# Performance work log

Hardware: AMD Instinct MI355X
Metric: run time of the kernel (lower is better)

The kernel has to match this reference:

```python
import jax, jax.numpy as jnp
import numpy as np

H, W, P, U = 32, 32, 64, 64
KB = KC = KD = 3
L, BSZ = 32, 8


def conv2d(x, k):
    # x: (N,H,W,Cin), k: (kh,kw,Cin,Cout), SAME padding, stride 1
    return jax.lax.conv_general_dilated(
        x, k, (1, 1), 'SAME', dimension_numbers=('NHWC', 'HWIO', 'NHWC'))


def dst_Q(N):
    # skew DST eigenbasis: Q[i,j] = i^(i+1) * sin(pi (i+1)(j+1)/(N+1)) / sqrt((N+1)/2)
    idx = jnp.arange(1, N + 1, dtype=jnp.float32)
    S = jnp.sin(jnp.pi * idx[:, None] * idx[None, :] / (N + 1)) / jnp.sqrt((N + 1) / 2.0)
    phase = jnp.exp(1j * (jnp.pi / 2.0) * idx)  # i^(i+1)
    return (phase[:, None] * S.astype(jnp.complex64)).astype(jnp.complex64)


def make_basis_skew(N, M):
    ih = jnp.arange(1, N + 1, dtype=jnp.float32)
    iw = jnp.arange(1, M + 1, dtype=jnp.float32)
    ch = 2.0 * jnp.cos(jnp.pi * ih / (N + 1))  # (N,)
    cw = 2.0 * jnp.cos(jnp.pi * iw / (M + 1))  # (M,)
    b = jnp.broadcast_to(cw[None, :], (N, M)).reshape(-1)
    c = jnp.broadcast_to(ch[:, None], (N, M)).reshape(-1)
    d = (ch[:, None] * cw[None, :]).reshape(-1)
    return jnp.stack((b, c, d), axis=-1)  # (N*M, 3)


def setup_inputs() -> dict:
    key = jax.random.key(0)
    ks = jax.random.split(key, 12)
    dt_min, dt_max = 0.001, 0.1
    inp = {
        'input_sequence': jax.random.normal(ks[0], (L, BSZ, H, W, U), dtype=jnp.float32),
        'x0': jax.random.normal(ks[1], (BSZ, H, W, U), dtype=jnp.float32),
        'Lambda_re': -(jax.random.uniform(ks[2], (P,), dtype=jnp.float32) * 0.9 + 0.1),
        'Lambda_im': jnp.pi * jnp.arange(P, dtype=jnp.float32),
        'values': jnp.zeros((P, 4), dtype=jnp.float32),
        'log_step': jax.random.uniform(ks[3], (P,), dtype=jnp.float32)
                    * (np.log(dt_max) - np.log(dt_min)) + np.log(dt_min),
        'B_r': jax.random.normal(ks[4], (KB, KB, U, P), dtype=jnp.float32) * np.sqrt(2.0 / (U * KB * KB)),
        'B_i': jax.random.normal(ks[5], (KB, KB, U, P), dtype=jnp.float32) * np.sqrt(2.0 / (U * KB * KB)),
        'C_r': jax.random.normal(ks[6], (KC, KC, P, U), dtype=jnp.float32) * np.sqrt(2.0 / (2 * P * KC * KC)),
        'C_i': jax.random.normal(ks[7], (KC, KC, P, U), dtype=jnp.float32) * np.sqrt(2.0 / (2 * P * KC * KC)),
        'D_kernel': jax.random.normal(ks[8], (KD, KD, U, U), dtype=jnp.float32) * np.sqrt(2.0 / (U * KD * KD)),
    }
    return inp


def reference(input_sequence, x0, Lambda_re, Lambda_im, values, log_step,
              B_r, B_i, C_r, C_i, D_kernel):
    Lq, Bq = input_sequence.shape[0], input_sequence.shape[1]
    # ---- diagonal state matrix (clip_eigs=True) ----
    Lambda = (jnp.minimum(Lambda_re, -1e-4) + 1j * Lambda_im).astype(jnp.complex64)  # (P,)
    # ---- diagonalized BTST spectrum D via skew basis ----
    basis = make_basis_skew(H, W).astype(jnp.complex64)  # (HW,3)
    v = jax.nn.softmax(values, axis=-1) * 4.0
    xk, yk, zk, wk = v[:, 0], v[:, 1], v[:, 2], v[:, 3]
    kv = jnp.stack(((xk + yk - 2) / 4, (xk + zk - 2) / 4, (xk + wk - 2) / 8), axis=-1).astype(jnp.complex64)
    D = jnp.einsum('pn,hn->ph', kv, basis) + 1.0  # (P, HW)
    # ---- ZOH discretization ----
    step = jnp.exp(log_step)  # (P,)
    temp = Lambda[:, None] * D  # (P, HW)
    A_bar = jnp.exp(temp * step[:, None])
    B_coeff = (A_bar - 1.0) / temp
    A_bar = A_bar.T.reshape(H, W, P)      # (H,W,P)
    B_coeff = B_coeff.T.reshape(H, W, P)  # (H,W,P)
    # ---- DST eigenbases ----
    Qh = dst_Q(H); Qw = dst_Q(W)
    Qh_inv = jnp.conj(Qh).T; Qw_inv = jnp.conj(Qw).T
    # ---- input path: B conv then transform to eigen domain ----
    u = input_sequence.reshape(Lq * Bq, H, W, U)
    Bu = (conv2d(u, B_r) + 1j * conv2d(u, B_i)).reshape(Lq, Bq, H, W, P)
    Bu_hat = jnp.einsum('ah,lbhwp,cw->lbacp', Qh_inv, Bu, Qw_inv)
    b_elems = B_coeff * Bu_hat  # (L,B,H,W,P)
    # ---- initial state from x0 through the same B path ----
    Bx0 = conv2d(x0, B_r) + 1j * conv2d(x0, B_i)  # (B,H,W,P)
    x0_hat = jnp.einsum('ah,bhwp,cw->bacp', Qh_inv, Bx0, Qw_inv) * B_coeff
    b_elems = b_elems.at[0].add(A_bar * x0_hat)
    # ---- parallel linear recurrence x_k = A_bar*x_{k-1} + b_k ----
    A_elems = jnp.broadcast_to(A_bar.astype(jnp.complex64), b_elems.shape)
    def binop(e1, e2):
        a1, b1 = e1; a2, b2 = e2
        return (a2 * a1, a2 * b1 + b2)
    _, xs = jax.lax.associative_scan(binop, (A_elems, b_elems), axis=0)
    # ---- back to spatial domain, C projection (2*Re), D feedthrough ----
    x_sp = jnp.einsum('ha,lbacp,wc->lbhwp', Qh, xs, Qw)  # (L,B,H,W,P) complex
    xr = x_sp.real.reshape(Lq * Bq, H, W, P)
    xi = x_sp.imag.reshape(Lq * Bq, H, W, P)
    y = 2.0 * (conv2d(xr, C_r) - conv2d(xi, C_i))  # Re(x @ C_tilde)
    y = y + conv2d(u, D_kernel)
    y = jax.nn.gelu(y)
    return y.reshape(Lq, Bq, H, W, U)
```

## Files before the change

kernel.cpp:

```cpp
#include <hip/hip_runtime.h>
#include <cmath>

#ifndef M_PI
#define M_PI 3.14159265358979323846
#endif

#define NH 32
#define NW 32
#define NP 64
#define NU 64
#define NL 32
#define NB 8
#define NIMG 256
#define NIMG_TOT 264
#define HWN 1024
#define IMG_STRIDE 65536

typedef unsigned short u16;
typedef unsigned int u32;
typedef __bf16 bf16x8 __attribute__((ext_vector_type(8)));
typedef float f32x4 __attribute__((ext_vector_type(4)));

__device__ __forceinline__ u16 f2bf(float f) {
  unsigned u = __float_as_uint(f);
  u += 0x7fffu + ((u >> 16) & 1u);
  return (u16)(u >> 16);
}
__device__ __forceinline__ float bf2f(u16 h) {
  return __uint_as_float(((unsigned)h) << 16);
}


__global__ void k_setup(const float* __restrict__ values, float* __restrict__ S,
                        float* __restrict__ kv) {
  int t = threadIdx.x;
  int i = t >> 5, j = t & 31;
  double s = sin(M_PI * (double)((i + 1) * (j + 1)) / 33.0) / sqrt(16.5);
  S[t] = (float)s;
  if (t < NP) {
    float v0 = values[t * 4 + 0], v1 = values[t * 4 + 1];
    float v2 = values[t * 4 + 2], v3 = values[t * 4 + 3];
    float m = fmaxf(fmaxf(v0, v1), fmaxf(v2, v3));
    float e0 = expf(v0 - m), e1 = expf(v1 - m), e2 = expf(v2 - m), e3 = expf(v3 - m);
    float inv = 4.0f / (e0 + e1 + e2 + e3);
    float xk = e0 * inv, yk = e1 * inv, zk = e2 * inv, wk = e3 * inv;
    kv[t * 4 + 0] = (xk + yk - 2.0f) * 0.25f;
    kv[t * 4 + 1] = (xk + zk - 2.0f) * 0.25f;
    kv[t * 4 + 2] = (xk + wk - 2.0f) * 0.125f;
    kv[t * 4 + 3] = 0.f;
  }
}

__global__ void k_coeff(const float* __restrict__ Lre, const float* __restrict__ Lim,
                        const float* __restrict__ log_step, const float* __restrict__ kv,
                        float2* __restrict__ A, float2* __restrict__ Bc) {
  int tid = blockIdx.x * blockDim.x + threadIdx.x;
  int n = tid >> 6, p = tid & 63;
  int h = n >> 5, w = n & 31;
  double ch = 2.0 * cos(M_PI * (double)(h + 1) / 33.0);
  double cw = 2.0 * cos(M_PI * (double)(w + 1) / 33.0);
  double Dv = (double)kv[p * 4 + 0] * cw + (double)kv[p * 4 + 1] * ch +
              (double)kv[p * 4 + 2] * ch * cw + 1.0;
  double lr = fmin((double)Lre[p], -0.0001);
  double li = (double)Lim[p];
  double tr = lr * Dv, ti = li * Dv;
  double st = exp((double)log_step[p]);
  double zr = tr * st, zi = ti * st;
  double ea = exp(zr);
  double Ar = ea * cos(zi), Ai = ea * sin(zi);
  double d = tr * tr + ti * ti;
  double br = ((Ar - 1.0) * tr + Ai * ti) / d;
  double bi = (Ai * tr - (Ar - 1.0) * ti) / d;
  size_t o = (size_t)(p >> 1) * 2048 + (size_t)n * 2 + (p & 1);
  A[o]  = make_float2((float)Ar, (float)Ai);
  Bc[o] = make_float2((float)br, (float)bi);
}

#define NB_PACK (18 * 8 * 64 * 8)
#define NC_PACK (54 * 4 * 64 * 8)
__global__ __launch_bounds__(256) void k_pack(
    const float* __restrict__ Br, const float* __restrict__ Bi,
    const float* __restrict__ Cr, const float* __restrict__ Ci,
    const float* __restrict__ Dk,
    u16* __restrict__ WBhi, u16* __restrict__ WBlo,
    u16* __restrict__ WChi, u16* __restrict__ WClo) {
  int tid = blockIdx.x * 256 + threadIdx.x;
  if (tid < NB_PACK) {
    int j = tid & 7, lane = (tid >> 3) & 63, nt = (tid >> 9) & 7, kc = tid >> 12;
    int k = kc * 32 + ((lane >> 4) << 3) + j;
    int n = nt * 16 + (lane & 15);
    int tap = k >> 6, c = k & 63;
    float w = (n < 64) ? Br[(tap * 64 + c) * 64 + n]
                       : Bi[(tap * 64 + c) * 64 + (n - 64)];
    u16 hi = f2bf(w);
    WBhi[tid] = hi;
    WBlo[tid] = f2bf(w - bf2f(hi));
  } else {
    int t2 = tid - NB_PACK;
    if (t2 < NC_PACK) {
      int j = t2 & 7, lane = (t2 >> 3) & 63, nt = (t2 >> 9) & 3, kc = t2 >> 11;
      int k = kc * 32 + ((lane >> 4) << 3) + j;
      int n = nt * 16 + (lane & 15);
      int s = k / 576, rem = k % 576;
      int tap = rem >> 6, c = rem & 63;
      int widx = (tap * 64 + c) * 64 + n;
      float w = (s == 0) ? 2.f * Cr[widx] : (s == 1) ? -2.f * Ci[widx] : Dk[widx];
      u16 hi = f2bf(w);
      WChi[t2] = hi;
      WClo[t2] = f2bf(w - bf2f(hi));
    }
  }
}

__global__ __launch_bounds__(256) void k_convB_mfma(
    const float* __restrict__ u, const float* __restrict__ x0,
    const u16* __restrict__ WBhi, const u16* __restrict__ WBlo,
    float2* __restrict__ XBUF) {
  __shared__ u16 lhs[6 * 34 * 64];
  __shared__ u16 lls[6 * 34 * 64];
  int img = blockIdx.x, h0 = blockIdx.y * 4;
  int t = threadIdx.x;
  const float* src = (img < NIMG) ? (u + (size_t)img * HWN * NU)
                                  : (x0 + (size_t)(img - NIMG) * HWN * NU);
  for (int z = t; z < 6 * 2 * 32; z += 256) {
    int col = z & 31, rw = z >> 5;
    int r = rw >> 1, w = (rw & 1) * 33;
    ((u32*)&lhs[(r * 34 + w) * 64])[col] = 0;
    ((u32*)&lls[(r * 34 + w) * 64])[col] = 0;
  }
  for (int idx = t; idx < 6 * 32 * 16; idx += 256) {
    int c4 = idx & 15, wi = (idx >> 4) & 31, r = idx >> 9;
    int hh = h0 - 1 + r;
    float4 v = make_float4(0.f, 0.f, 0.f, 0.f);
    if (hh >= 0 && hh < NH)
      v = *(const float4*)(src + (hh * 32 + wi) * 64 + c4 * 4);
    u16 a0 = f2bf(v.x), a1 = f2bf(v.y), a2 = f2bf(v.z), a3 = f2bf(v.w);
    u16 b0 = f2bf(v.x - bf2f(a0)), b1 = f2bf(v.y - bf2f(a1));
    u16 b2 = f2bf(v.z - bf2f(a2)), b3 = f2bf(v.w - bf2f(a3));
    int w = wi + 1;
    int a = (r * 34 + w) * 64 + (((c4 >> 1) ^ (w & 7)) << 3) + ((c4 & 1) << 2);
    *(ushort4*)&lhs[a] = make_ushort4(a0, a1, a2, a3);
    *(ushort4*)&lls[a] = make_ushort4(b0, b1, b2, b3);
  }
  __syncthreads();
  int lane = t & 63, wv = t >> 6;
  int mgrp = wv >> 1, ng = wv & 1;
  int l15 = lane & 15, l4 = lane >> 4;
  f32x4 acc[4][4];
#pragma unroll
  for (int i = 0; i < 4; i++)
#pragma unroll
    for (int q = 0; q < 4; q++) acc[i][q] = (f32x4){0.f, 0.f, 0.f, 0.f};

  for (int tap = 0; tap < 9; tap++) {
    int kh = tap / 3, kw = tap - kh * 3;
#pragma unroll
    for (int cc = 0; cc < 2; cc++) {
      int kc = tap * 2 + cc;
      bf16x8 ah[4], al[4], wh[4], wl[4];
#pragma unroll
      for (int mti = 0; mti < 4; mti++) {
        int row = mgrp * 2 + (mti >> 1);
        int wt = (mti & 1) * 16 + l15 + kw;
        int off = ((row + kh) * 34 + wt) * 64 + (((cc * 4 + l4) ^ (wt & 7)) << 3);
        ah[mti] = *(const bf16x8*)&lhs[off];
        al[mti] = *(const bf16x8*)&lls[off];
      }
#pragma unroll
      for (int q = 0; q < 4; q++) {
        int nt = ng * 2 + (q & 1) + (q >> 1) * 4;
        size_t woff = ((size_t)((kc * 8 + nt) * 64 + lane)) * 8;
        wh[q] = *(const bf16x8*)&WBhi[woff];
        wl[q] = *(const bf16x8*)&WBlo[woff];
      }
#pragma unroll
      for (int mti = 0; mti < 4; mti++)
#pragma unroll
        for (int q = 0; q < 4; q++) {
          f32x4 c = acc[mti][q];
          c = __builtin_amdgcn_mfma_f32_16x16x32_bf16(ah[mti], wh[q], c, 0, 0, 0);
          c = __builtin_amdgcn_mfma_f32_16x16x32_bf16(ah[mti], wl[q], c, 0, 0, 0);
          c = __builtin_amdgcn_mfma_f32_16x16x32_bf16(al[mti], wh[q], c, 0, 0, 0);
          acc[mti][q] = c;
        }
    }
  }
  float2* dst = XBUF + (size_t)img * IMG_STRIDE;
#pragma unroll
  for (int mti = 0; mti < 4; mti++) {
    int h = h0 + mgrp * 2 + (mti >> 1);
#pragma unroll
    for (int half = 0; half < 2; half++) {
      int p = ng * 32 + half * 16 + l15;
      int pc = p >> 1, pp = p & 1;
#pragma unroll
      for (int reg = 0; reg < 4; reg++) {
        int wpix = (mti & 1) * 16 + l4 * 4 + reg;
        float re = acc[mti][half][reg];
        float im = acc[mti][2 + half][reg];
        int m = (h + wpix + 2) & 3;
        float2 o;
        if (m == 0)      o = make_float2( re,  im);
        else if (m == 1) o = make_float2( im, -re);
        else if (m == 2) o = make_float2(-re, -im);
        else             o = make_float2(-im,  re);
        dst[(size_t)pc * 2048 + (h * 32 + wpix) * 2 + pp] = o;
      }
    }
  }
}

__global__ __launch_bounds__(256) void k_dst_fwd(float2* __restrict__ XBUF,
                                                 const float* __restrict__ S) {
  int img = blockIdx.x, pc = blockIdx.y;
  __shared__ float tin[32 * 32 * 4];
  __shared__ float t1 [32 * 32 * 4];
  int t = threadIdx.x;
  float2* base = XBUF + (size_t)img * IMG_STRIDE + (size_t)pc * 2048;
  for (int n = t; n < 1024; n += 256) {
    float4 v = *(const float4*)&base[n * 2];
    *(float4*)&tin[n * 4] = v;
  }
  __syncthreads();
  {
    int w = t & 31, ag = t >> 5;
    f32x4 acc[4];
#pragma unroll
    for (int i = 0; i < 4; i++) acc[i] = (f32x4){0.f, 0.f, 0.f, 0.f};
#pragma unroll 8
    for (int hh = 0; hh < 32; hh++) {
      f32x4 v = *(const f32x4*)&tin[(hh * 32 + w) * 4];
      f32x4 s4 = *(const f32x4*)&S[hh * 32 + ag * 4];
#pragma unroll
      for (int i = 0; i < 4; i++) acc[i] += s4[i] * v;
    }
    int wp = w ^ (ag & 7);
#pragma unroll
    for (int i = 0; i < 4; i++)
      *(f32x4*)&t1[((ag * 4 + i) * 32 + wp) * 4] = acc[i];
  }
  __syncthreads();
  {
    int pp = t & 1, cg = (t >> 1) & 15, ag = t >> 5;
    float acc[4][2][2];
#pragma unroll
    for (int i = 0; i < 4; i++)
#pragma unroll
      for (int j = 0; j < 2; j++) acc[i][j][0] = acc[i][j][1] = 0.f;
#pragma unroll 8
    for (int w = 0; w < 32; w++) {
      int wp = w ^ (ag & 7);
      float2 sc = *(const float2*)&S[w * 32 + cg * 2];
#pragma unroll
      for (int i = 0; i < 4; i++) {
        float2 tv = *(const float2*)&t1[((ag * 4 + i) * 32 + wp) * 4 + pp * 2];
        acc[i][0][0] = fmaf(tv.x, sc.x, acc[i][0][0]);
        acc[i][0][1] = fmaf(tv.y, sc.x, acc[i][0][1]);
        acc[i][1][0] = fmaf(tv.x, sc.y, acc[i][1][0]);
        acc[i][1][1] = fmaf(tv.y, sc.y, acc[i][1][1]);
      }
    }
#pragma unroll
    for (int i = 0; i < 4; i++)
#pragma unroll
      for (int j = 0; j < 2; j++) {
        int n = (ag * 4 + i) * 32 + cg * 2 + j;
        base[n * 2 + pp] = make_float2(acc[i][j][0], acc[i][j][1]);
      }
  }
}

__global__ __launch_bounds__(256) void k_scan(const float2* __restrict__ A,
                                              const float2* __restrict__ Bc,
                                              float2* __restrict__ X) {
  int gx = blockIdx.x;
  int b = gx >> 8, sl = gx & 255;
  int t = threadIdx.x;
  size_t off = (size_t)sl * 256 + t;
  float2 Av = A[off];
  float2 Bv = Bc[off];
  float2 v0 = X[(size_t)(NIMG + b) * IMG_STRIDE + off];
  float2 x;
  x.x = Bv.x * v0.x - Bv.y * v0.y;
  x.y = Bv.x * v0.y + Bv.y * v0.x;
#pragma unroll 4
  for (int l = 0; l < NL; l++) {
    size_t idx = (size_t)(l * NB + b) * IMG_STRIDE + off;
    float2 v = X[idx];
    float vr = Bv.x * v.x - Bv.y * v.y;
    float vi = Bv.x * v.y + Bv.y * v.x;
    float2 nx;
    nx.x = Av.x * x.x - Av.y * x.y + vr;
    nx.y = Av.x * x.y + Av.y * x.x + vi;
    x = nx;
    X[idx] = x;
  }
}

__global__ __launch_bounds__(256) void k_dst_inv(float2* __restrict__ XBUF,
                                                 const float* __restrict__ S) {
  int img = blockIdx.x, pc = blockIdx.y;
  __shared__ float tin[32 * 32 * 4];
  __shared__ float t1 [32 * 32 * 4];
  int t = threadIdx.x;
  float2* base = XBUF + (size_t)img * IMG_STRIDE + (size_t)pc * 2048;
  for (int n = t; n < 1024; n += 256) {
    float4 v = *(const float4*)&base[n * 2];
    *(float4*)&tin[n * 4] = v;
  }
  __syncthreads();
  {
    int c = t & 31, ag = t >> 5;
    f32x4 acc[4];
#pragma unroll
    for (int i = 0; i < 4; i++) acc[i] = (f32x4){0.f, 0.f, 0.f, 0.f};
#pragma unroll 8
    for (int a = 0; a < 32; a++) {
      f32x4 v = *(const f32x4*)&tin[(a * 32 + c) * 4];
      f32x4 s4 = *(const f32x4*)&S[a * 32 + ag * 4];
#pragma unroll
      for (int i = 0; i < 4; i++) acc[i] += s4[i] * v;
    }
    int cp = c ^ (ag & 7);
#pragma unroll
    for (int i = 0; i < 4; i++)
      *(f32x4*)&t1[((ag * 4 + i) * 32 + cp) * 4] = acc[i];
  }
  __syncthreads();
  {
    int pp = t & 1, wg = (t >> 1) & 15, ag = t >> 5;
    float acc[4][2][2];
#pragma unroll
    for (int i = 0; i < 4; i++)
#pragma unroll
      for (int j = 0; j < 2; j++) acc[i][j][0] = acc[i][j][1] = 0.f;
#pragma unroll 8
    for (int c = 0; c < 32; c++) {
      int cp = c ^ (ag & 7);
      float2 sc = *(const float2*)&S[c * 32 + wg * 2];
#pragma unroll
      for (int i = 0; i < 4; i++) {
        float2 tv = *(const float2*)&t1[((ag * 4 + i) * 32 + cp) * 4 + pp * 2];
        acc[i][0][0] = fmaf(tv.x, sc.x, acc[i][0][0]);
        acc[i][0][1] = fmaf(tv.y, sc.x, acc[i][0][1]);
        acc[i][1][0] = fmaf(tv.x, sc.y, acc[i][1][0]);
        acc[i][1][1] = fmaf(tv.y, sc.y, acc[i][1][1]);
      }
    }
    u32* gw = (u32*)(XBUF + (size_t)img * IMG_STRIDE) + (size_t)pc * 4096;
#pragma unroll
    for (int i = 0; i < 4; i++)
#pragma unroll
      for (int j = 0; j < 2; j++) {
        int h = ag * 4 + i, wpx = wg * 2 + j;
        float re = acc[i][j][0], im = acc[i][j][1];
        int m = (h + wpx + 2) & 3;
        float2 o;
        if (m == 0)      o = make_float2( re,  im);
        else if (m == 1) o = make_float2(-im,  re);
        else if (m == 2) o = make_float2(-re, -im);
        else             o = make_float2( im, -re);
        u16 hr = f2bf(o.x), lr = f2bf(o.x - bf2f(hr));
        u16 hm = f2bf(o.y), lm = f2bf(o.y - bf2f(hm));
        int pix = h * 32 + wpx;
        gw[pix * 4 + pp]     = (u32)hr | ((u32)lr << 16);
        gw[pix * 4 + 2 + pp] = (u32)hm | ((u32)lm << 16);
      }
  }
}

__global__ __launch_bounds__(256) void k_convCD_mfma(
    const u32* __restrict__ XP,
    const float* __restrict__ u,
    const u16* __restrict__ WChi, const u16* __restrict__ WClo,
    float* __restrict__ out) {
  __shared__ u16 lhs[6 * 34 * 64];
  __shared__ u16 lls[6 * 34 * 64];
  int img = blockIdx.x, h0 = blockIdx.y * 4;
  int t = threadIdx.x;
  int lane = t & 63, wv = t >> 6;
  int mgrp = wv >> 1, ng = wv & 1;
  int l15 = lane & 15, l4 = lane >> 4;
  const u32* xim = XP + (size_t)img * IMG_STRIDE * 2;
  const float* uim = u + (size_t)img * HWN * NU;
  f32x4 acc[4][2];
#pragma unroll
  for (int i = 0; i < 4; i++) {
    acc[i][0] = (f32x4){0.f, 0.f, 0.f, 0.f};
    acc[i][1] = (f32x4){0.f, 0.f, 0.f, 0.f};
  }
  for (int z = t; z < 6 * 2 * 32; z += 256) {
    int col = z & 31, rw = z >> 5;
    int r = rw >> 1, w = (rw & 1) * 33;
    ((u32*)&lhs[(r * 34 + w) * 64])[col] = 0;
    ((u32*)&lls[(r * 34 + w) * 64])[col] = 0;
  }

  for (int s = 0; s < 3; s++) {
    __syncthreads();
    if (s < 2) {
      for (int idx = t; idx < 6 * 32 * 32; idx += 256) {
        int wi = idx & 31, pc = (idx >> 5) & 31, r = idx >> 10;
        int hh = h0 - 1 + r;
        uint2 d = make_uint2(0u, 0u);
        if (hh >= 0 && hh < NH)
          d = *(const uint2*)(xim + (size_t)pc * 4096 + (hh * 32 + wi) * 4 + s * 2);
        u32 hip = (d.x & 0xffffu) | (d.y << 16);
        u32 lop = (d.x >> 16) | (d.y & 0xffff0000u);
        int w = wi + 1;
        int c = pc * 2;
        int a = (r * 34 + w) * 64 + (((c >> 3) ^ (w & 7)) << 3) + (c & 7);
        *(u32*)&lhs[a] = hip;
        *(u32*)&lls[a] = lop;
      }
    } else {
      for (int idx = t; idx < 6 * 32 * 16; idx += 256) {
        int c4 = idx & 15, wi = (idx >> 4) & 31, r = idx >> 9;
        int hh = h0 - 1 + r;
        float4 v = make_float4(0.f, 0.f, 0.f, 0.f);
        if (hh >= 0 && hh < NH)
          v = *(const float4*)(uim + (hh * 32 + wi) * 64 + c4 * 4);
        u16 a0 = f2bf(v.x), a1 = f2bf(v.y), a2 = f2bf(v.z), a3 = f2bf(v.w);
        u16 b0 = f2bf(v.x - bf2f(a0)), b1 = f2bf(v.y - bf2f(a1));
        u16 b2 = f2bf(v.z - bf2f(a2)), b3 = f2bf(v.w - bf2f(a3));
        int w = wi + 1;
        int a = (r * 34 + w) * 64 + (((c4 >> 1) ^ (w & 7)) << 3) + ((c4 & 1) << 2);
        *(ushort4*)&lhs[a] = make_ushort4(a0, a1, a2, a3);
        *(ushort4*)&lls[a] = make_ushort4(b0, b1, b2, b3);
      }
    }
    __syncthreads();
    for (int tap = 0; tap < 9; tap++) {
      int kh = tap / 3, kw = tap - kh * 3;
#pragma unroll
      for (int cc = 0; cc < 2; cc++) {
        int kc = (s * 9 + tap) * 2 + cc;
        bf16x8 ah[4], al[4], wh[2], wl[2];
#pragma unroll
        for (int mti = 0; mti < 4; mti++) {
          int row = mgrp * 2 + (mti >> 1);
          int wt = (mti & 1) * 16 + l15 + kw;
          int off = ((row + kh) * 34 + wt) * 64 + (((cc * 4 + l4) ^ (wt & 7)) << 3);
          ah[mti] = *(const bf16x8*)&lhs[off];
          al[mti] = *(const bf16x8*)&lls[off];
        }
#pragma unroll
        for (int q = 0; q < 2; q++) {
          int nt = ng * 2 + q;
          size_t woff = ((size_t)((kc * 4 + nt) * 64 + lane)) * 8;
          wh[q] = *(const bf16x8*)&WChi[woff];
          wl[q] = *(const bf16x8*)&WClo[woff];
        }
#pragma unroll
        for (int mti = 0; mti < 4; mti++)
#pragma unroll
          for (int q = 0; q < 2; q++) {
            f32x4 c = acc[mti][q];
            c = __builtin_amdgcn_mfma_f32_16x16x32_bf16(ah[mti], wh[q], c, 0, 0, 0);
            c = __builtin_amdgcn_mfma_f32_16x16x32_bf16(ah[mti], wl[q], c, 0, 0, 0);
            c = __builtin_amdgcn_mfma_f32_16x16x32_bf16(al[mti], wh[q], c, 0, 0, 0);
            acc[mti][q] = c;
          }
      }
    }
  }
  float* dst = out + (size_t)img * HWN * NU;
#pragma unroll
  for (int mti = 0; mti < 4; mti++) {
    int h = h0 + mgrp * 2 + (mti >> 1);
#pragma unroll
    for (int q = 0; q < 2; q++) {
      int un = (ng * 2 + q) * 16 + l15;
#pragma unroll
      for (int reg = 0; reg < 4; reg++) {
        int wpix = (mti & 1) * 16 + l4 * 4 + reg;
        float x = acc[mti][q][reg];
        float z = 0.7978845608028654f * (x + 0.044715f * x * x * x);
        float e = __expf(2.f * z);
        float th = 1.f - 2.f / (e + 1.f);
        dst[(h * 32 + wpix) * 64 + un] = 0.5f * x * (1.f + th);
      }
    }
  }
}

extern "C" void kernel_launch(void* const* d_in, const int* in_sizes, int n_in,
                              void* d_out, int out_size, void* d_ws, size_t ws_size,
                              hipStream_t stream) {
  const float* u        = (const float*)d_in[0];
  const float* x0       = (const float*)d_in[1];
  const float* Lre      = (const float*)d_in[2];
  const float* Lim      = (const float*)d_in[3];
  const float* values   = (const float*)d_in[4];
  const float* log_step = (const float*)d_in[5];
  const float* Br       = (const float*)d_in[6];
  const float* Bi       = (const float*)d_in[7];
  const float* Cr       = (const float*)d_in[8];
  const float* Ci       = (const float*)d_in[9];
  const float* Dk       = (const float*)d_in[10];
  float* out = (float*)d_out;

  char* ws = (char*)d_ws;
  float*  S    = (float*)ws;                       ws += 4096;
  float*  kv   = (float*)ws;                       ws += 4096;
  float2* A    = (float2*)ws;                      ws += 524288;
  float2* Bc   = (float2*)ws;                      ws += 524288;
  u16*    WBhi = (u16*)ws;                         ws += NB_PACK * 2;
  u16*    WBlo = (u16*)ws;                         ws += NB_PACK * 2;
  u16*    WChi = (u16*)ws;                         ws += NC_PACK * 2;
  u16*    WClo = (u16*)ws;                         ws += NC_PACK * 2;
  float2* XBUF = (float2*)ws;

  hipLaunchKernelGGL(k_setup,      dim3(1),            dim3(1024), 0, stream, values, S, kv);
  hipLaunchKernelGGL(k_coeff,      dim3(256),          dim3(256),  0, stream, Lre, Lim, log_step, kv, A, Bc);
  hipLaunchKernelGGL(k_pack,       dim3(720),          dim3(256),  0, stream, Br, Bi, Cr, Ci, Dk, WBhi, WBlo, WChi, WClo);
  hipLaunchKernelGGL(k_convB_mfma, dim3(NIMG_TOT, 8),  dim3(256),  0, stream, u, x0, WBhi, WBlo, XBUF);
  hipLaunchKernelGGL(k_dst_fwd,    dim3(NIMG_TOT, 32), dim3(256),  0, stream, XBUF, S);
  hipLaunchKernelGGL(k_scan,       dim3(2048),         dim3(256),  0, stream, A, Bc, XBUF);
  hipLaunchKernelGGL(k_dst_inv,    dim3(NIMG, 32),     dim3(256),  0, stream, XBUF, S);
  hipLaunchKernelGGL(k_convCD_mfma,dim3(NIMG, 8),      dim3(256),  0, stream, (const u32*)XBUF, u, WChi, WClo, out);
}
```

Measured before the change: 653.8 us.

## Switch C/D conv to 32x32x16 MFMA with channel-blocked LDS layout

Rewrites the C/D projection convolution to use 32x32x16 bf16 MFMA tiles instead of 16x16x32. The weight packing and the LDS activation layout change to match: channels are grouped in blocks of 8 with no XOR swizzle, and the GELU epilogue is remapped. Each wave now does fewer, larger MFMAs per weight load, and the kernel gets a launch-bounds occupancy hint. The B conv also precomputes its swizzled LDS offsets outside the tap loop. The unswizzled layout risks LDS bank conflicts.

New measurement: 685.5 us. 1.05x slower.

```diff
diff --git a/kernel.cpp b/kernel.cpp
--- a/kernel.cpp
+++ b/kernel.cpp
@@ -20,6 +20,7 @@
 typedef unsigned int u32;
 typedef __bf16 bf16x8 __attribute__((ext_vector_type(8)));
 typedef float f32x4 __attribute__((ext_vector_type(4)));
+typedef float f32x16 __attribute__((ext_vector_type(16)));
 
 __device__ __forceinline__ u16 f2bf(float f) {
   unsigned u = __float_as_uint(f);
@@ -77,7 +78,7 @@
 }
 
 #define NB_PACK (18 * 8 * 64 * 8)
-#define NC_PACK (54 * 4 * 64 * 8)
+#define NC_PACK (108 * 2 * 64 * 8)
 __global__ __launch_bounds__(256) void k_pack(
     const float* __restrict__ Br, const float* __restrict__ Bi,
     const float* __restrict__ Cr, const float* __restrict__ Ci,
@@ -98,11 +99,13 @@
   } else {
     int t2 = tid - NB_PACK;
     if (t2 < NC_PACK) {
-      int j = t2 & 7, lane = (t2 >> 3) & 63, nt = (t2 >> 9) & 3, kc = t2 >> 11;
-      int k = kc * 32 + ((lane >> 4) << 3) + j;
-      int n = nt * 16 + (lane & 15);
+      int j = t2 & 7, lane = (t2 >> 3) & 63, nt = (t2 >> 9) & 1, kk = t2 >> 10;
+      int ch = (kk & 3) * 16 + (lane >> 5) * 8 + j;
+      int stap = kk >> 2;
+      int k = stap * 64 + ch;
       int s = k / 576, rem = k % 576;
       int tap = rem >> 6, c = rem & 63;
+      int n = nt * 32 + (lane & 31);
       int widx = (tap * 64 + c) * 64 + n;
       float w = (s == 0) ? 2.f * Cr[widx] : (s == 1) ? -2.f * Ci[widx] : Dk[widx];
       u16 hi = f2bf(w);
@@ -146,6 +149,16 @@
   int lane = t & 63, wv = t >> 6;
   int mgrp = wv >> 1, ng = wv & 1;
   int l15 = lane & 15, l4 = lane >> 4;
+  int swz[2][3][2];
+#pragma unroll
+  for (int p = 0; p < 2; p++)
+#pragma unroll
+    for (int kw = 0; kw < 3; kw++) {
+      int wt = p * 16 + l15 + kw;
+#pragma unroll
+      for (int cc = 0; cc < 2; cc++)
+        swz[p][kw][cc] = wt * 64 + (((cc * 4 + l4) ^ (wt & 7)) << 3);
+    }
   f32x4 acc[4][4];
 #pragma unroll
   for (int i = 0; i < 4; i++)
@@ -161,8 +174,7 @@
 #pragma unroll
       for (int mti = 0; mti < 4; mti++) {
         int row = mgrp * 2 + (mti >> 1);
-        int wt = (mti & 1) * 16 + l15 + kw;
-        int off = ((row + kh) * 34 + wt) * 64 + (((cc * 4 + l4) ^ (wt & 7)) << 3);
+        int off = (row + kh) * 2176 + swz[mti & 1][kw][cc];
         ah[mti] = *(const bf16x8*)&lhs[off];
         al[mti] = *(const bf16x8*)&lls[off];
       }
@@ -369,37 +381,35 @@
   }
 }
 
-__global__ __launch_bounds__(256) void k_convCD_mfma(
+__global__ __launch_bounds__(256, 3) void k_convCD_mfma(
     const u32* __restrict__ XP,
     const float* __restrict__ u,
     const u16* __restrict__ WChi, const u16* __restrict__ WClo,
     float* __restrict__ out) {
-  __shared__ u16 lhs[6 * 34 * 64];
-  __shared__ u16 lls[6 * 34 * 64];
+  __shared__ u16 lhs[8 * 6 * 34 * 8];
+  __shared__ u16 lls[8 * 6 * 34 * 8];
   int img = blockIdx.x, h0 = blockIdx.y * 4;
   int t = threadIdx.x;
   int lane = t & 63, wv = t >> 6;
-  int mgrp = wv >> 1, ng = wv & 1;
-  int l15 = lane & 15, l4 = lane >> 4;
+  int mp = wv >> 1, n = wv & 1;
+  int hi = lane >> 5, l31 = lane & 31;
   const u32* xim = XP + (size_t)img * IMG_STRIDE * 2;
   const float* uim = u + (size_t)img * HWN * NU;
-  f32x4 acc[4][2];
-#pragma unroll
-  for (int i = 0; i < 4; i++) {
-    acc[i][0] = (f32x4){0.f, 0.f, 0.f, 0.f};
-    acc[i][1] = (f32x4){0.f, 0.f, 0.f, 0.f};
-  }
-  for (int z = t; z < 6 * 2 * 32; z += 256) {
-    int col = z & 31, rw = z >> 5;
-    int r = rw >> 1, w = (rw & 1) * 33;
-    ((u32*)&lhs[(r * 34 + w) * 64])[col] = 0;
-    ((u32*)&lls[(r * 34 + w) * 64])[col] = 0;
-  }
+  f32x16 acc0, acc1;
+#pragma unroll
+  for (int i = 0; i < 16; i++) { acc0[i] = 0.f; acc1[i] = 0.f; }
+  for (int z = t; z < 8 * 6 * 2 * 4; z += 256) {
+    int col = z & 3, rest = z >> 2;
+    int w = (rest & 1) * 33, gr = rest >> 1;
+    ((u32*)lhs)[(gr * 34 + w) * 4 + col] = 0;
+    ((u32*)lls)[(gr * 34 + w) * 4 + col] = 0;
+  }
+  int pbase = hi * 1632 + l31 * 8 + mp * 544;
 
   for (int s = 0; s < 3; s++) {
     __syncthreads();
     if (s < 2) {
-      for (int idx = t; idx < 6 * 32 * 32; idx += 256) {
+      for (int idx = t; idx < 6144; idx += 256) {
         int wi = idx & 31, pc = (idx >> 5) & 31, r = idx >> 10;
         int hh = h0 - 1 + r;
         uint2 d = make_uint2(0u, 0u);
@@ -407,14 +417,12 @@
           d = *(const uint2*)(xim + (size_t)pc * 4096 + (hh * 32 + wi) * 4 + s * 2);
         u32 hip = (d.x & 0xffffu) | (d.y << 16);
         u32 lop = (d.x >> 16) | (d.y & 0xffff0000u);
-        int w = wi + 1;
-        int c = pc * 2;
-        int a = (r * 34 + w) * 64 + (((c >> 3) ^ (w & 7)) << 3) + (c & 7);
+        int a = (((pc >> 2) * 6 + r) * 34 + wi + 1) * 8 + (pc & 3) * 2;
         *(u32*)&lhs[a] = hip;
         *(u32*)&lls[a] = lop;
       }
     } else {
-      for (int idx = t; idx < 6 * 32 * 16; idx += 256) {
+      for (int idx = t; idx < 3072; idx += 256) {
         int c4 = idx & 15, wi = (idx >> 4) & 31, r = idx >> 9;
         int hh = h0 - 1 + r;
         float4 v = make_float4(0.f, 0.f, 0.f, 0.f);
@@ -423,63 +431,50 @@
         u16 a0 = f2bf(v.x), a1 = f2bf(v.y), a2 = f2bf(v.z), a3 = f2bf(v.w);
         u16 b0 = f2bf(v.x - bf2f(a0)), b1 = f2bf(v.y - bf2f(a1));
         u16 b2 = f2bf(v.z - bf2f(a2)), b3 = f2bf(v.w - bf2f(a3));
-        int w = wi + 1;
-        int a = (r * 34 + w) * 64 + (((c4 >> 1) ^ (w & 7)) << 3) + ((c4 & 1) << 2);
+        int a = (((c4 >> 1) * 6 + r) * 34 + wi + 1) * 8 + (c4 & 1) * 4;
         *(ushort4*)&lhs[a] = make_ushort4(a0, a1, a2, a3);
         *(ushort4*)&lls[a] = make_ushort4(b0, b1, b2, b3);
       }
     }
     __syncthreads();
-    for (int tap = 0; tap < 9; tap++) {
-      int kh = tap / 3, kw = tap - kh * 3;
-#pragma unroll
-      for (int cc = 0; cc < 2; cc++) {
-        int kc = (s * 9 + tap) * 2 + cc;
-        bf16x8 ah[4], al[4], wh[2], wl[2];
-#pragma unroll
-        for (int mti = 0; mti < 4; mti++) {
-          int row = mgrp * 2 + (mti >> 1);
-          int wt = (mti & 1) * 16 + l15 + kw;
-          int off = ((row + kh) * 34 + wt) * 64 + (((cc * 4 + l4) ^ (wt & 7)) << 3);
-          ah[mti] = *(const bf16x8*)&lhs[off];
-          al[mti] = *(const bf16x8*)&lls[off];
+    for (int kh = 0; kh < 3; kh++) {
+      int rbase = pbase + kh * 272;
+#pragma unroll
+      for (int kw = 0; kw < 3; kw++)
+#pragma unroll
+        for (int ki = 0; ki < 4; ki++) {
+          int kk = (s * 9 + kh * 3 + kw) * 4 + ki;
+          int o0 = rbase + ki * 3264 + kw * 8;
+          int o1 = o0 + 272;
+          bf16x8 ah0 = *(const bf16x8*)&lhs[o0];
+          bf16x8 al0 = *(const bf16x8*)&lls[o0];
+          bf16x8 ah1 = *(const bf16x8*)&lhs[o1];
+          bf16x8 al1 = *(const bf16x8*)&lls[o1];
+          size_t woff = ((size_t)((kk * 2 + n) * 64 + lane)) * 8;
+          bf16x8 wh = *(const bf16x8*)&WChi[woff];
+          bf16x8 wl = *(const bf16x8*)&WClo[woff];
+          acc0 = __builtin_amdgcn_mfma_f32_32x32x16_bf16(ah0, wh, acc0, 0, 0, 0);
+          acc0 = __builtin_amdgcn_mfma_f32_32x32x16_bf16(ah0, wl, acc0, 0, 0, 0);
+          acc0 = __builtin_amdgcn_mfma_f32_32x32x16_bf16(al0, wh, acc0, 0, 0, 0);
+          acc1 = __builtin_amdgcn_mfma_f32_32x32x16_bf16(ah1, wh, acc1, 0, 0, 0);
+          acc1 = __builtin_amdgcn_mfma_f32_32x32x16_bf16(ah1, wl, acc1, 0, 0, 0);
+          acc1 = __builtin_amdgcn_mfma_f32_32x32x16_bf16(al1, wh, acc1, 0, 0, 0);
         }
-#pragma unroll
-        for (int q = 0; q < 2; q++) {
-          int nt = ng * 2 + q;
-          size_t woff = ((size_t)((kc * 4 + nt) * 64 + lane)) * 8;
-          wh[q] = *(const bf16x8*)&WChi[woff];
-          wl[q] = *(const bf16x8*)&WClo[woff];
-        }
-#pragma unroll
-        for (int mti = 0; mti < 4; mti++)
-#pragma unroll
-          for (int q = 0; q < 2; q++) {
-            f32x4 c = acc[mti][q];
-            c = __builtin_amdgcn_mfma_f32_16x16x32_bf16(ah[mti], wh[q], c, 0, 0, 0);
-            c = __builtin_amdgcn_mfma_f32_16x16x32_bf16(ah[mti], wl[q], c, 0, 0, 0);
-            c = __builtin_amdgcn_mfma_f32_16x16x32_bf16(al[mti], wh[q], c, 0, 0, 0);
-            acc[mti][q] = c;
-          }
-      }
     }
   }
   float* dst = out + (size_t)img * HWN * NU;
-#pragma unroll
-  for (int mti = 0; mti < 4; mti++) {
-    int h = h0 + mgrp * 2 + (mti >> 1);
-#pragma unroll
-    for (int q = 0; q < 2; q++) {
-      int un = (ng * 2 + q) * 16 + l15;
-#pragma unroll
-      for (int reg = 0; reg < 4; reg++) {
-        int wpix = (mti & 1) * 16 + l4 * 4 + reg;
-        float x = acc[mti][q][reg];
-        float z = 0.7978845608028654f * (x + 0.044715f * x * x * x);
-        float e = __expf(2.f * z);
-        float th = 1.f - 2.f / (e + 1.f);
-        dst[(h * 32 + wpix) * 64 + un] = 0.5f * x * (1.f + th);
-      }
+  int un = n * 32 + l31;
+#pragma unroll
+  for (int m01 = 0; m01 < 2; m01++) {
+    int h = h0 + mp * 2 + m01;
+#pragma unroll
+    for (int reg = 0; reg < 16; reg++) {
+      int wpix = (reg & 3) + 8 * (reg >> 2) + 4 * hi;
+      float x = (m01 == 0) ? acc0[reg] : acc1[reg];
+      float z = 0.7978845608028654f * (x + 0.044715f * x * x * x);
+      float e = __expf(2.f * z);
+      float th = 1.f - 2.f / (e + 1.f);
+      dst[(h * 32 + wpix) * 64 + un] = 0.5f * x * (1.f + th);
     }
   }
 }
```
